# Kernel tuning notes

Measured on AMD Instinct MI355X. Metric: run time of the kernel, lower is better.

## Reference

```python
import jax, jax.numpy as jnp
import numpy as np


def setup_inputs() -> dict:
    key = jax.random.key(0)
    k1, k2, k3, k4 = jax.random.split(key, 4)
    L, T, D = 8192, 8192, 1024
    return {
        "x": jax.random.normal(k1, (L, D), dtype=jnp.float32),
        "Wq": jax.random.normal(k2, (D, D), dtype=jnp.float32) / np.sqrt(D),
        "Pk": jax.random.normal(k3, (1, T, D), dtype=jnp.float32),
        "Pv": jax.random.normal(k4, (1, T, D), dtype=jnp.float32),
        "sliding_window_size": 512,
    }


def reference(x, Wq, Pk, Pv, sliding_window_size):
    # x: (L, d); Pk/Pv: (1, T, d); single-head cross attention with
    # bidirectional sliding-window mask |q_idx - kv_idx| < window.
    L, d = x.shape
    k = Pk[0]  # (T, d)
    v = Pv[0]  # (T, d)
    q = x @ Wq.T  # torch Linear (bias-free): y = x W^T
    scale = d ** -0.5  # flex_attention default scale
    scores = jnp.einsum("qd,td->qt", q, k) * scale  # (L, T)
    q_idx = jnp.arange(L)[:, None]
    kv_idx = jnp.arange(k.shape[0])[None, :]
    mask = jnp.abs(q_idx - kv_idx) < sliding_window_size
    scores = jnp.where(mask, scores, -jnp.inf)
    attn = jax.nn.softmax(scores, axis=-1)
    y = attn @ v  # (L, d)
    return y[None]  # (1, L, d) matching y.squeeze(1) of (1,1,L,d)
```

## Files before the change

### kernel.cpp

```cpp
#include <hip/hip_runtime.h>
#include <hip/hip_bf16.h>
#include <stdint.h>
#include <stddef.h>


typedef __bf16 bf16x8 __attribute__((ext_vector_type(8)));
typedef __bf16 bf16x4 __attribute__((ext_vector_type(4)));
typedef float  f32x4  __attribute__((ext_vector_type(4)));

constexpr int Lq   = 8192;
constexpr int Tk   = 8192;
constexpr int Dd   = 1024;
constexpr int WINW = 512;
constexpr int NQT  = 64;
constexpr int BAND = 1152;
constexpr int VTP  = 9344;

constexpr size_t OFF_XB  = 0;
constexpr size_t OFF_WQB = OFF_XB  + (size_t)Lq * Dd * 2;
constexpr size_t OFF_QB  = OFF_WQB + (size_t)Dd * Dd * 2;
constexpr size_t OFF_KB  = OFF_QB  + (size_t)Lq * Dd * 2;
constexpr size_t OFF_VT  = OFF_KB  + (size_t)Tk * Dd * 2;
constexpr size_t OFF_RS  = OFF_VT  + (size_t)Dd * VTP * 2;
constexpr size_t OFF_P   = OFF_RS  + (size_t)Lq * 4;
constexpr size_t WS_NEED = OFF_P   + (size_t)Lq * BAND * 2;

__device__ __forceinline__ void gload_lds16(const void* g, void* l) {
    __builtin_amdgcn_global_load_lds(
        (const __attribute__((address_space(1))) void*)g,
        (__attribute__((address_space(3))) void*)l, 16, 0, 0);
}

__device__ __forceinline__ int xcd_swz(int bid, int cpx) {
    return (bid & 7) * cpx + (bid >> 3);
}

__device__ __forceinline__ void gemm_core(const __bf16* __restrict__ A, int lda,
                                          const __bf16* __restrict__ B, int ldb,
                                          int nK, f32x4 acc[4][4],
                                          __bf16* As, __bf16* Bs)
{
    const int tid  = threadIdx.x;
    const int wid  = tid >> 6;
    const int lane = tid & 63;
    const int wm   = wid >> 1, wn = wid & 1;
    const int srow = lane >> 2;
    const int scol = (lane & 3) * 8;
    const int fr   = lane & 15;
    const int kq   = (lane >> 4) * 8;

#pragma unroll
    for (int m = 0; m < 4; ++m)
#pragma unroll
        for (int n = 0; n < 4; ++n)
            acc[m][n] = 0.f;

    auto stage = [&](int k0, int buf) {
#pragma unroll
        for (int j = 0; j < 2; ++j) {
            const int r = 32 * wid + 16 * j + srow;
            __bf16* da = As + buf * 4096 + (32 * wid + 16 * j) * 32;
            __bf16* db = Bs + buf * 4096 + (32 * wid + 16 * j) * 32;
            gload_lds16(A + (size_t)r * lda + (k0 + scol), da);
            gload_lds16(B + (size_t)r * ldb + (k0 + scol), db);
        }
    };

    stage(0, 0);
    __syncthreads();
    int cur = 0;
    const int nt = nK >> 5;
    for (int t = 0; t < nt; ++t) {
        if (t + 1 < nt) stage((t + 1) << 5, cur ^ 1);
        const __bf16* Ab = As + cur * 4096;
        const __bf16* Bb = Bs + cur * 4096;
        bf16x8 a[4], b[4];
#pragma unroll
        for (int m = 0; m < 4; ++m)
            a[m] = *(const bf16x8*)(Ab + (64 * wm + 16 * m + fr) * 32 + kq);
#pragma unroll
        for (int n = 0; n < 4; ++n)
            b[n] = *(const bf16x8*)(Bb + (64 * wn + 16 * n + fr) * 32 + kq);
#pragma unroll
        for (int m = 0; m < 4; ++m)
#pragma unroll
            for (int n = 0; n < 4; ++n)
                acc[m][n] = __builtin_amdgcn_mfma_f32_16x16x32_bf16(a[m], b[n], acc[m][n], 0, 0, 0);
        __syncthreads();
        cur ^= 1;
    }
}

__global__ __launch_bounds__(256) void kcvt_all(const float* __restrict__ x,
                                                const float* __restrict__ wq,
                                                const float* __restrict__ pk,
                                                __bf16* __restrict__ xb,
                                                __bf16* __restrict__ wqb,
                                                __bf16* __restrict__ kb,
                                                float* __restrict__ rs)
{
    const int gid = blockIdx.x * 256 + threadIdx.x;
    const int stride = gridDim.x * 256;
    if (gid < Lq / 4) ((uint4*)rs)[gid] = uint4{0u, 0u, 0u, 0u};
    constexpr int NX4 = Lq * Dd / 4, NW4 = Dd * Dd / 4, NK4 = Tk * Dd / 4;
    for (int i = gid; i < NX4; i += stride) {
        const float4 v = *(const float4*)(x + (size_t)i * 4);
        *(bf16x4*)(xb + (size_t)i * 4) = bf16x4{(__bf16)v.x, (__bf16)v.y, (__bf16)v.z, (__bf16)v.w};
    }
    for (int i = gid; i < NW4; i += stride) {
        const float4 v = *(const float4*)(wq + (size_t)i * 4);
        *(bf16x4*)(wqb + (size_t)i * 4) = bf16x4{(__bf16)v.x, (__bf16)v.y, (__bf16)v.z, (__bf16)v.w};
    }
    for (int i = gid; i < NK4; i += stride) {
        const float4 v = *(const float4*)(pk + (size_t)i * 4);
        *(bf16x4*)(kb + (size_t)i * 4) = bf16x4{(__bf16)v.x, (__bf16)v.y, (__bf16)v.z, (__bf16)v.w};
    }
}

__global__ __launch_bounds__(256) void kzero16(uint4* __restrict__ dst, int n)
{
    int i = blockIdx.x * 256 + threadIdx.x;
    const int stride = gridDim.x * 256;
    const uint4 z = {0u, 0u, 0u, 0u};
    for (; i < n; i += stride) dst[i] = z;
}

__global__ __launch_bounds__(256) void ktransV(const float* __restrict__ V,
                                               __bf16* __restrict__ Vt)
{
    __shared__ float tile[64][65];
    const int kv0 = blockIdx.y * 64, d0 = blockIdx.x * 64;
    const int tid = threadIdx.x;
    const int r = tid >> 4, c = (tid & 15) * 4;
#pragma unroll
    for (int ph = 0; ph < 4; ++ph) {
        const float4 v = *(const float4*)(V + (size_t)(kv0 + 16 * ph + r) * Dd + d0 + c);
        tile[16 * ph + r][c + 0] = v.x;
        tile[16 * ph + r][c + 1] = v.y;
        tile[16 * ph + r][c + 2] = v.z;
        tile[16 * ph + r][c + 3] = v.w;
    }
    __syncthreads();
#pragma unroll
    for (int ph = 0; ph < 4; ++ph) {
        const int dr = 16 * ph + r;
        bf16x4 o = {(__bf16)tile[c + 0][dr], (__bf16)tile[c + 1][dr],
                    (__bf16)tile[c + 2][dr], (__bf16)tile[c + 3][dr]};
        *(bf16x4*)(Vt + (size_t)(d0 + dr) * VTP + 512 + kv0 + c) = o;
    }
}

__global__ __launch_bounds__(256) void kqgemm(const __bf16* __restrict__ xb,
                                              const __bf16* __restrict__ wqb,
                                              __bf16* __restrict__ qb)
{
    __shared__ __bf16 As[2 * 128 * 32], Bs[2 * 128 * 32];
    const int swz = xcd_swz(blockIdx.x, 64);
    const int mt = swz >> 3, nt = swz & 7;
    f32x4 acc[4][4];
    gemm_core(xb + (size_t)mt * 128 * Dd, Dd, wqb + (size_t)nt * 128 * Dd, Dd, Dd, acc, As, Bs);

    const int lane = threadIdx.x & 63, wid = threadIdx.x >> 6;
    const int wm = wid >> 1, wn = wid & 1;
    const int rb = (lane >> 4) * 4, cb = lane & 15;
#pragma unroll
    for (int m = 0; m < 4; ++m)
#pragma unroll
        for (int n = 0; n < 4; ++n)
#pragma unroll
            for (int r = 0; r < 4; ++r) {
                const int row = mt * 128 + 64 * wm + 16 * m + rb + r;
                const int col = nt * 128 + 64 * wn + 16 * n + cb;
                qb[(size_t)row * Dd + col] = (__bf16)acc[m][n][r];
            }
}

__global__ __launch_bounds__(256) void ksgemm(const __bf16* __restrict__ qb,
                                              const __bf16* __restrict__ kb,
                                              __bf16* __restrict__ Pp,
                                              float* __restrict__ rs)
{
    __shared__ __bf16 As[2 * 128 * 32], Bs[2 * 128 * 32];
    const int swz = xcd_swz(blockIdx.x, 72);
    const int t = swz / 9, jb = swz - 9 * t;
    const int kvbase = 128 * t - 512 + 128 * jb;
    f32x4 acc[4][4];
    gemm_core(qb + (size_t)t * 128 * Dd, Dd, kb + (ptrdiff_t)kvbase * Dd, Dd, Dd, acc, As, Bs);

    const int lane = threadIdx.x & 63, wid = threadIdx.x >> 6;
    const int wm = wid >> 1, wn = wid & 1;
    const int rb = (lane >> 4) * 4, cb = lane & 15;
    const float scale = 0.03125f;
#pragma unroll
    for (int m = 0; m < 4; ++m)
#pragma unroll
        for (int r = 0; r < 4; ++r) {
            const int rl = 64 * wm + 16 * m + rb + r;
            const int q  = 128 * t + rl;
            float rsum = 0.f;
#pragma unroll
            for (int n = 0; n < 4; ++n) {
                const int cl = 64 * wn + 16 * n + cb;
                const int kv = kvbase + cl;
                const int dd = q - kv;
                const bool ok = (kv >= 0) && (kv < Tk) && (dd < WINW) && (dd > -WINW);
                const float e = ok ? __expf(acc[m][n][r] * scale) : 0.f;
                Pp[(size_t)q * BAND + 128 * jb + cl] = (__bf16)e;
                rsum += e;
            }
#pragma unroll
            for (int off = 1; off < 16; off <<= 1) rsum += __shfl_xor(rsum, off);
            if (cb == 0) atomicAdd(&rs[q], rsum);
        }
}

__global__ __launch_bounds__(256) void kpvgemm(const __bf16* __restrict__ Pp,
                                               const __bf16* __restrict__ Vt,
                                               const float* __restrict__ rs,
                                               float* __restrict__ out)
{
    __shared__ __bf16 As[2 * 128 * 32], Bs[2 * 128 * 32];
    const int swz = xcd_swz(blockIdx.x, 64);
    const int t = swz >> 3, nb = swz & 7;
    f32x4 acc[4][4];
    gemm_core(Pp + (size_t)t * 128 * BAND, BAND,
              Vt + (size_t)nb * 128 * VTP + 128 * t, VTP, BAND, acc, As, Bs);

    const int lane = threadIdx.x & 63, wid = threadIdx.x >> 6;
    const int wm = wid >> 1, wn = wid & 1;
    const int rb = (lane >> 4) * 4, cb = lane & 15;
#pragma unroll
    for (int m = 0; m < 4; ++m)
#pragma unroll
        for (int r = 0; r < 4; ++r) {
            const int row = 128 * t + 64 * wm + 16 * m + rb + r;
            const float inv = 1.f / rs[row];
#pragma unroll
            for (int n = 0; n < 4; ++n) {
                const int col = 128 * nb + 64 * wn + 16 * n + cb;
                out[(size_t)row * Dd + col] = acc[m][n][r] * inv;
            }
        }
}

extern "C" void kernel_launch(void* const* d_in, const int* in_sizes, int n_in,
                              void* d_out, int out_size, void* d_ws, size_t ws_size,
                              hipStream_t stream)
{
    const float* x  = (const float*)d_in[0];
    const float* Wq = (const float*)d_in[1];
    const float* Pk = (const float*)d_in[2];
    const float* Pv = (const float*)d_in[3];
    float* out = (float*)d_out;

    if (ws_size < WS_NEED) return;

    char* ws = (char*)d_ws;
    __bf16* xb  = (__bf16*)(ws + OFF_XB);
    __bf16* wqb = (__bf16*)(ws + OFF_WQB);
    __bf16* qb  = (__bf16*)(ws + OFF_QB);
    __bf16* kb  = (__bf16*)(ws + OFF_KB);
    __bf16* vt  = (__bf16*)(ws + OFF_VT);
    float*  rs  = (float*)(ws + OFF_RS);
    __bf16* Pp  = (__bf16*)(ws + OFF_P);

    kcvt_all<<<2048, 256, 0, stream>>>(x, Wq, Pk, xb, wqb, kb, rs);
    kzero16<<<2048, 256, 0, stream>>>((uint4*)vt, (int)((size_t)Dd * VTP * 2 / 16));
    ktransV<<<dim3(Dd / 64, Tk / 64), 256, 0, stream>>>(Pv, vt);

    kqgemm<<<512, 256, 0, stream>>>(xb, wqb, qb);
    ksgemm<<<576, 256, 0, stream>>>(qb, kb, Pp, rs);
    kpvgemm<<<512, 256, 0, stream>>>(Pp, vt, rs, out);
}
```

Measured before the change: 252.5 us.

## Use 8 waves per GEMM block and fold V-pad zeroing into convert kernel

The three 128x128 GEMM kernels now launch 512 threads (8 waves), each wave computing a 32x64 sub-tile, with one 16-byte load per thread per stage. This halves per-wave accumulator registers and adds more waves for latency hiding, at the cost of less per-wave operand reuse. The separate zero kernel for the whole transposed-V buffer is removed. Only the pad columns are now zeroed, inside the conversion kernel, which saves one launch and most of a large memset.

```diff
diff --git a/kernel.cpp b/kernel.cpp
--- a/kernel.cpp
+++ b/kernel.cpp
@@ -35,35 +35,32 @@
     return (bid & 7) * cpx + (bid >> 3);
 }
 
-__device__ __forceinline__ void gemm_core(const __bf16* __restrict__ A, int lda,
-                                          const __bf16* __restrict__ B, int ldb,
-                                          int nK, f32x4 acc[4][4],
-                                          __bf16* As, __bf16* Bs)
+__device__ __forceinline__ void gemm_core8(const __bf16* __restrict__ A, int lda,
+                                           const __bf16* __restrict__ B, int ldb,
+                                           int nK, f32x4 acc[2][4],
+                                           __bf16* As, __bf16* Bs)
 {
     const int tid  = threadIdx.x;
     const int wid  = tid >> 6;
     const int lane = tid & 63;
-    const int wm   = wid >> 1, wn = wid & 1;
-    const int srow = lane >> 2;
-    const int scol = (lane & 3) * 8;
+    const int wm   = wid >> 1;
+    const int wn   = wid & 1;
+    const int srow = tid >> 2;
+    const int scol = (tid & 3) * 8;
     const int fr   = lane & 15;
     const int kq   = (lane >> 4) * 8;
 
 #pragma unroll
-    for (int m = 0; m < 4; ++m)
+    for (int m = 0; m < 2; ++m)
 #pragma unroll
         for (int n = 0; n < 4; ++n)
             acc[m][n] = 0.f;
 
     auto stage = [&](int k0, int buf) {
-#pragma unroll
-        for (int j = 0; j < 2; ++j) {
-            const int r = 32 * wid + 16 * j + srow;
-            __bf16* da = As + buf * 4096 + (32 * wid + 16 * j) * 32;
-            __bf16* db = Bs + buf * 4096 + (32 * wid + 16 * j) * 32;
-            gload_lds16(A + (size_t)r * lda + (k0 + scol), da);
-            gload_lds16(B + (size_t)r * ldb + (k0 + scol), db);
-        }
+        __bf16* da = As + buf * 4096 + (wid << 9);
+        __bf16* db = Bs + buf * 4096 + (wid << 9);
+        gload_lds16(A + (size_t)srow * lda + (k0 + scol), da);
+        gload_lds16(B + (size_t)srow * ldb + (k0 + scol), db);
     };
 
     stage(0, 0);
@@ -74,15 +71,15 @@
         if (t + 1 < nt) stage((t + 1) << 5, cur ^ 1);
         const __bf16* Ab = As + cur * 4096;
         const __bf16* Bb = Bs + cur * 4096;
-        bf16x8 a[4], b[4];
-#pragma unroll
-        for (int m = 0; m < 4; ++m)
-            a[m] = *(const bf16x8*)(Ab + (64 * wm + 16 * m + fr) * 32 + kq);
+        bf16x8 a[2], b[4];
+#pragma unroll
+        for (int m = 0; m < 2; ++m)
+            a[m] = *(const bf16x8*)(Ab + (32 * wm + 16 * m + fr) * 32 + kq);
 #pragma unroll
         for (int n = 0; n < 4; ++n)
             b[n] = *(const bf16x8*)(Bb + (64 * wn + 16 * n + fr) * 32 + kq);
 #pragma unroll
-        for (int m = 0; m < 4; ++m)
+        for (int m = 0; m < 2; ++m)
 #pragma unroll
             for (int n = 0; n < 4; ++n)
                 acc[m][n] = __builtin_amdgcn_mfma_f32_16x16x32_bf16(a[m], b[n], acc[m][n], 0, 0, 0);
@@ -97,11 +94,19 @@
                                                 __bf16* __restrict__ xb,
                                                 __bf16* __restrict__ wqb,
                                                 __bf16* __restrict__ kb,
+                                                uint4* __restrict__ vt4,
                                                 float* __restrict__ rs)
 {
     const int gid = blockIdx.x * 256 + threadIdx.x;
     const int stride = gridDim.x * 256;
-    if (gid < Lq / 4) ((uint4*)rs)[gid] = uint4{0u, 0u, 0u, 0u};
+    const uint4 z = {0u, 0u, 0u, 0u};
+    if (gid < Lq / 4) ((uint4*)rs)[gid] = z;
+    constexpr int NPAD = Dd * 144;
+    for (int i = gid; i < NPAD; i += stride) {
+        const int row = i / 144, j = i - row * 144;
+        const int ch = (j < 64) ? j : (j + 1024);
+        vt4[(size_t)row * 1168 + ch] = z;
+    }
     constexpr int NX4 = Lq * Dd / 4, NW4 = Dd * Dd / 4, NK4 = Tk * Dd / 4;
     for (int i = gid; i < NX4; i += stride) {
         const float4 v = *(const float4*)(x + (size_t)i * 4);
@@ -115,14 +120,6 @@
         const float4 v = *(const float4*)(pk + (size_t)i * 4);
         *(bf16x4*)(kb + (size_t)i * 4) = bf16x4{(__bf16)v.x, (__bf16)v.y, (__bf16)v.z, (__bf16)v.w};
     }
-}
-
-__global__ __launch_bounds__(256) void kzero16(uint4* __restrict__ dst, int n)
-{
-    int i = blockIdx.x * 256 + threadIdx.x;
-    const int stride = gridDim.x * 256;
-    const uint4 z = {0u, 0u, 0u, 0u};
-    for (; i < n; i += stride) dst[i] = z;
 }
 
 __global__ __launch_bounds__(256) void ktransV(const float* __restrict__ V,
@@ -150,32 +147,32 @@
     }
 }
 
-__global__ __launch_bounds__(256) void kqgemm(const __bf16* __restrict__ xb,
+__global__ __launch_bounds__(512) void kqgemm(const __bf16* __restrict__ xb,
                                               const __bf16* __restrict__ wqb,
                                               __bf16* __restrict__ qb)
 {
     __shared__ __bf16 As[2 * 128 * 32], Bs[2 * 128 * 32];
     const int swz = xcd_swz(blockIdx.x, 64);
     const int mt = swz >> 3, nt = swz & 7;
-    f32x4 acc[4][4];
-    gemm_core(xb + (size_t)mt * 128 * Dd, Dd, wqb + (size_t)nt * 128 * Dd, Dd, Dd, acc, As, Bs);
+    f32x4 acc[2][4];
+    gemm_core8(xb + (size_t)mt * 128 * Dd, Dd, wqb + (size_t)nt * 128 * Dd, Dd, Dd, acc, As, Bs);
 
     const int lane = threadIdx.x & 63, wid = threadIdx.x >> 6;
     const int wm = wid >> 1, wn = wid & 1;
     const int rb = (lane >> 4) * 4, cb = lane & 15;
 #pragma unroll
-    for (int m = 0; m < 4; ++m)
+    for (int m = 0; m < 2; ++m)
 #pragma unroll
         for (int n = 0; n < 4; ++n)
 #pragma unroll
             for (int r = 0; r < 4; ++r) {
-                const int row = mt * 128 + 64 * wm + 16 * m + rb + r;
+                const int row = mt * 128 + 32 * wm + 16 * m + rb + r;
                 const int col = nt * 128 + 64 * wn + 16 * n + cb;
                 qb[(size_t)row * Dd + col] = (__bf16)acc[m][n][r];
             }
 }
 
-__global__ __launch_bounds__(256) void ksgemm(const __bf16* __restrict__ qb,
+__global__ __launch_bounds__(512) void ksgemm(const __bf16* __restrict__ qb,
                                               const __bf16* __restrict__ kb,
                                               __bf16* __restrict__ Pp,
                                               float* __restrict__ rs)
@@ -184,18 +181,18 @@
     const int swz = xcd_swz(blockIdx.x, 72);
     const int t = swz / 9, jb = swz - 9 * t;
     const int kvbase = 128 * t - 512 + 128 * jb;
-    f32x4 acc[4][4];
-    gemm_core(qb + (size_t)t * 128 * Dd, Dd, kb + (ptrdiff_t)kvbase * Dd, Dd, Dd, acc, As, Bs);
+    f32x4 acc[2][4];
+    gemm_core8(qb + (size_t)t * 128 * Dd, Dd, kb + (ptrdiff_t)kvbase * Dd, Dd, Dd, acc, As, Bs);
 
     const int lane = threadIdx.x & 63, wid = threadIdx.x >> 6;
     const int wm = wid >> 1, wn = wid & 1;
     const int rb = (lane >> 4) * 4, cb = lane & 15;
     const float scale = 0.03125f;
 #pragma unroll
-    for (int m = 0; m < 4; ++m)
+    for (int m = 0; m < 2; ++m)
 #pragma unroll
         for (int r = 0; r < 4; ++r) {
-            const int rl = 64 * wm + 16 * m + rb + r;
+            const int rl = 32 * wm + 16 * m + rb + r;
             const int q  = 128 * t + rl;
             float rsum = 0.f;
 #pragma unroll
@@ -214,7 +211,7 @@
         }
 }
 
-__global__ __launch_bounds__(256) void kpvgemm(const __bf16* __restrict__ Pp,
+__global__ __launch_bounds__(512) void kpvgemm(const __bf16* __restrict__ Pp,
                                                const __bf16* __restrict__ Vt,
                                                const float* __restrict__ rs,
                                                float* __restrict__ out)
@@ -222,18 +219,18 @@
     __shared__ __bf16 As[2 * 128 * 32], Bs[2 * 128 * 32];
     const int swz = xcd_swz(blockIdx.x, 64);
     const int t = swz >> 3, nb = swz & 7;
-    f32x4 acc[4][4];
-    gemm_core(Pp + (size_t)t * 128 * BAND, BAND,
-              Vt + (size_t)nb * 128 * VTP + 128 * t, VTP, BAND, acc, As, Bs);
+    f32x4 acc[2][4];
+    gemm_core8(Pp + (size_t)t * 128 * BAND, BAND,
+               Vt + (size_t)nb * 128 * VTP + 128 * t, VTP, BAND, acc, As, Bs);
 
     const int lane = threadIdx.x & 63, wid = threadIdx.x >> 6;
     const int wm = wid >> 1, wn = wid & 1;
     const int rb = (lane >> 4) * 4, cb = lane & 15;
 #pragma unroll
-    for (int m = 0; m < 4; ++m)
+    for (int m = 0; m < 2; ++m)
 #pragma unroll
         for (int r = 0; r < 4; ++r) {
-            const int row = 128 * t + 64 * wm + 16 * m + rb + r;
+            const int row = 128 * t + 32 * wm + 16 * m + rb + r;
             const float inv = 1.f / rs[row];
 #pragma unroll
             for (int n = 0; n < 4; ++n) {
@@ -264,11 +261,10 @@
     float*  rs  = (float*)(ws + OFF_RS);
     __bf16* Pp  = (__bf16*)(ws + OFF_P);
 
-    kcvt_all<<<2048, 256, 0, stream>>>(x, Wq, Pk, xb, wqb, kb, rs);
-    kzero16<<<2048, 256, 0, stream>>>((uint4*)vt, (int)((size_t)Dd * VTP * 2 / 16));
+    kcvt_all<<<2048, 256, 0, stream>>>(x, Wq, Pk, xb, wqb, kb, (uint4*)vt, rs);
     ktransV<<<dim3(Dd / 64, Tk / 64), 256, 0, stream>>>(Pv, vt);
 
-    kqgemm<<<512, 256, 0, stream>>>(xb, wqb, qb);
-    ksgemm<<<576, 256, 0, stream>>>(qb, kb, Pp, rs);
-    kpvgemm<<<512, 256, 0, stream>>>(Pp, vt, rs, out);
-}
+    kqgemm<<<512, 512, 0, stream>>>(xb, wqb, qb);
+    ksgemm<<<576, 512, 0, stream>>>(qb, kb, Pp, rs);
+    kpvgemm<<<512, 512, 0, stream>>>(Pp, vt, rs, out);
+}
```

After: 233.0 us. 1.08x faster.
